# Optimization experiments

Measured on AMD Instinct MI355X. Metric: run time of the kernel, lower is better.

Reference implementation:

```python
import jax, jax.numpy as jnp
import numpy as np

N_NODES = 100000
N_EDGES = 1600000
IN_F = 256
OUT_F = 64


def setup_inputs() -> dict:
    key = jax.random.key(0)
    k1, k2, k3, k4, k5, k6 = jax.random.split(key, 6)
    x = jax.random.normal(k1, (N_NODES, IN_F), dtype=jnp.float32)
    edge_vals = jax.random.uniform(k2, (N_EDGES,), dtype=jnp.float32)
    W = jax.random.normal(k3, (IN_F, OUT_F), dtype=jnp.float32) * (1.0 / np.sqrt(OUT_F))
    bias = jax.random.normal(k4, (OUT_F,), dtype=jnp.float32) * (1.0 / np.sqrt(OUT_F))
    row_idx = jnp.sort(jax.random.randint(k5, (N_EDGES,), 0, N_NODES, dtype=jnp.int32))
    col_idx = jax.random.randint(k6, (N_EDGES,), 0, N_NODES, dtype=jnp.int32)
    return {"x": x, "edge_vals": edge_vals, "W": W, "bias": bias,
            "row_idx": row_idx, "col_idx": col_idx}


def reference(x, edge_vals, W, bias, row_idx, col_idx):
    # support = X @ W  (dense GEMM; torch.mm / torch.spmm branch)
    support = x @ W                                  # [N, OUT_F]
    # flexspmm: output = A @ support, A given as weighted edge list
    msgs = support[col_idx] * edge_vals[:, None]      # [E, OUT_F] gather + scale
    out = jax.ops.segment_sum(msgs, row_idx, num_segments=x.shape[0])  # [N, OUT_F]
    return out + bias
```

## Files before the change

kernel.cpp:

```cpp
#include <hip/hip_runtime.h>
#include <hip/hip_bf16.h>

#define N_NODES 100000
#define N_EDGES 1600000
#define IN_F 256
#define OUT_F 64

typedef short bf16x8 __attribute__((ext_vector_type(8)));
typedef float f32x4 __attribute__((ext_vector_type(4)));

__device__ __forceinline__ short f2bf(float f) {
  unsigned u = __float_as_uint(f);
  u += 0x7FFF + ((u >> 16) & 1);
  return (short)(u >> 16);
}
__device__ __forceinline__ float bf2f(unsigned short u) {
  return __uint_as_float(((unsigned)u) << 16);
}

__global__ __launch_bounds__(256) void build_row_ptr_kernel(
    const int* __restrict__ row_idx, int* __restrict__ row_ptr) {
  int i = blockIdx.x * blockDim.x + threadIdx.x;
  if (i > N_NODES) return;
  int lo = 0, hi = N_EDGES;
  while (lo < hi) {
    int mid = (lo + hi) >> 1;
    if (row_idx[mid] < i) lo = mid + 1; else hi = mid;
  }
  row_ptr[i] = lo;
}

__global__ __launch_bounds__(256) void wfrag_kernel(
    const float* __restrict__ W, short* __restrict__ Wf) {
  int tid = blockIdx.x * blockDim.x + threadIdx.x;
  if (tid >= 2048) return;
  int s = tid >> 8;
  int r = tid & 255;
  int t = r >> 6;
  int lane = r & 63;
  int col = t * 16 + (lane & 15);
  int kbase = s * 32 + ((lane >> 4) & 3) * 8;
#pragma unroll
  for (int j = 0; j < 8; ++j) {
    Wf[(size_t)tid * 8 + j] = f2bf(W[(size_t)(kbase + j) * OUT_F + col]);
  }
}

__global__ __launch_bounds__(256) void gemm_kernel(
    const float* __restrict__ x, const short* __restrict__ Wf,
    unsigned short* __restrict__ supB) {
  __shared__ short sWf[8 * 4 * 64 * 8];
  {
    const float4* g = reinterpret_cast<const float4*>(Wf);
    float4* s4 = reinterpret_cast<float4*>(sWf);
#pragma unroll
    for (int i = 0; i < 8; ++i) s4[threadIdx.x + i * 256] = g[threadIdx.x + i * 256];
  }
  __syncthreads();

  const int lane = threadIdx.x & 63;
  const int wave = threadIdx.x >> 6;
  const int r0_base = blockIdx.x * 64 + wave * 16;

  int arow = r0_base + (lane & 15);
  if (arow >= N_NODES) arow = N_NODES - 1;
  const float* xrow = x + (size_t)arow * IN_F + ((lane >> 4) & 3) * 8;

  f32x4 acc0 = {0.f, 0.f, 0.f, 0.f};
  f32x4 acc1 = {0.f, 0.f, 0.f, 0.f};
  f32x4 acc2 = {0.f, 0.f, 0.f, 0.f};
  f32x4 acc3 = {0.f, 0.f, 0.f, 0.f};

#pragma unroll
  for (int s = 0; s < 8; ++s) {
    const float4 f0 = *reinterpret_cast<const float4*>(xrow + s * 32);
    const float4 f1 = *reinterpret_cast<const float4*>(xrow + s * 32 + 4);
    bf16x8 a;
    a[0] = f2bf(f0.x); a[1] = f2bf(f0.y); a[2] = f2bf(f0.z); a[3] = f2bf(f0.w);
    a[4] = f2bf(f1.x); a[5] = f2bf(f1.y); a[6] = f2bf(f1.z); a[7] = f2bf(f1.w);
    const bf16x8 b0 = *reinterpret_cast<const bf16x8*>(&sWf[((s * 4 + 0) * 64 + lane) * 8]);
    const bf16x8 b1 = *reinterpret_cast<const bf16x8*>(&sWf[((s * 4 + 1) * 64 + lane) * 8]);
    const bf16x8 b2 = *reinterpret_cast<const bf16x8*>(&sWf[((s * 4 + 2) * 64 + lane) * 8]);
    const bf16x8 b3 = *reinterpret_cast<const bf16x8*>(&sWf[((s * 4 + 3) * 64 + lane) * 8]);
    acc0 = __builtin_amdgcn_mfma_f32_16x16x32_bf16(a, b0, acc0, 0, 0, 0);
    acc1 = __builtin_amdgcn_mfma_f32_16x16x32_bf16(a, b1, acc1, 0, 0, 0);
    acc2 = __builtin_amdgcn_mfma_f32_16x16x32_bf16(a, b2, acc2, 0, 0, 0);
    acc3 = __builtin_amdgcn_mfma_f32_16x16x32_bf16(a, b3, acc3, 0, 0, 0);
  }

  const int orow_base = r0_base + ((lane >> 4) & 3) * 4;
  const int ocol = lane & 15;
#pragma unroll
  for (int r = 0; r < 4; ++r) {
    const int row = orow_base + r;
    if (row < N_NODES) {
      unsigned short* o = supB + (size_t)row * OUT_F + ocol;
      o[0]  = (unsigned short)f2bf(acc0[r]);
      o[16] = (unsigned short)f2bf(acc1[r]);
      o[32] = (unsigned short)f2bf(acc2[r]);
      o[48] = (unsigned short)f2bf(acc3[r]);
    }
  }
}

__global__ __launch_bounds__(256) void spmm_kernel(
    const unsigned short* __restrict__ supB, const float* __restrict__ ev,
    const int* __restrict__ col, const int* __restrict__ row_ptr,
    const float* __restrict__ bias, float* __restrict__ out) {
  const int lane = threadIdx.x & 63;
  const int g = lane >> 4;
  const int fq = lane & 15;
  const int gwave = (blockIdx.x * blockDim.x + threadIdx.x) >> 6;
  const int nwaves = (gridDim.x * blockDim.x) >> 6;

  const float b0 = bias[fq * 4 + 0];
  const float b1 = bias[fq * 4 + 1];
  const float b2 = bias[fq * 4 + 2];
  const float b3 = bias[fq * 4 + 3];

  for (int node = gwave; node < N_NODES; node += nwaves) {
    const int s = row_ptr[node];
    const int e = row_ptr[node + 1];
    float a0 = 0.f, a1 = 0.f, a2 = 0.f, a3 = 0.f;

    for (int i = s; i < e; i += 8) {
      const int i0 = i + g;
      const int i1 = i + 4 + g;
      const bool p0 = i0 < e;
      const bool p1 = i1 < e;
      const int c0 = p0 ? col[i0] : 0;
      const int c1 = p1 ? col[i1] : 0;
      const float v0 = p0 ? ev[i0] : 0.f;
      const float v1 = p1 ? ev[i1] : 0.f;
      const ushort4 s0 = *reinterpret_cast<const ushort4*>(supB + (size_t)c0 * OUT_F + fq * 4);
      const ushort4 s1 = *reinterpret_cast<const ushort4*>(supB + (size_t)c1 * OUT_F + fq * 4);
      a0 = fmaf(v0, bf2f(s0.x), a0);
      a1 = fmaf(v0, bf2f(s0.y), a1);
      a2 = fmaf(v0, bf2f(s0.z), a2);
      a3 = fmaf(v0, bf2f(s0.w), a3);
      a0 = fmaf(v1, bf2f(s1.x), a0);
      a1 = fmaf(v1, bf2f(s1.y), a1);
      a2 = fmaf(v1, bf2f(s1.z), a2);
      a3 = fmaf(v1, bf2f(s1.w), a3);
    }

    a0 += __shfl_xor(a0, 16); a0 += __shfl_xor(a0, 32);
    a1 += __shfl_xor(a1, 16); a1 += __shfl_xor(a1, 32);
    a2 += __shfl_xor(a2, 16); a2 += __shfl_xor(a2, 32);
    a3 += __shfl_xor(a3, 16); a3 += __shfl_xor(a3, 32);

    if (lane < 16) {
      float4 o;
      o.x = a0 + b0; o.y = a1 + b1; o.z = a2 + b2; o.w = a3 + b3;
      *reinterpret_cast<float4*>(out + (size_t)node * OUT_F + fq * 4) = o;
    }
  }
}

extern "C" void kernel_launch(void* const* d_in, const int* in_sizes, int n_in,
                              void* d_out, int out_size, void* d_ws, size_t ws_size,
                              hipStream_t stream) {
  const float* x        = (const float*)d_in[0];
  const float* ev       = (const float*)d_in[1];
  const float* W        = (const float*)d_in[2];
  const float* bias     = (const float*)d_in[3];
  const int*   row_idx  = (const int*)d_in[4];
  const int*   col_idx  = (const int*)d_in[5];
  float* out = (float*)d_out;

  int*            row_ptr = (int*)d_ws;
  short*          Wf      = (short*)((char*)d_ws + 448 * 1024);
  unsigned short* supB    = (unsigned short*)((char*)d_ws + 512 * 1024);

  build_row_ptr_kernel<<<(N_NODES + 1 + 255) / 256, 256, 0, stream>>>(row_idx, row_ptr);
  wfrag_kernel<<<8, 256, 0, stream>>>(W, Wf);

  gemm_kernel<<<(N_NODES + 63) / 64, 256, 0, stream>>>(x, Wf, supB);

  spmm_kernel<<<2048, 256, 0, stream>>>(supB, ev, col_idx, row_ptr, bias, out);
}
```

Baseline: 79.44 us.

## Process two nodes per wave iteration with contiguous node ranges and nontemporal loads

The SpMM kernel now gives each wave a contiguous block of nodes instead of a strided assignment. It processes two adjacent rows at once, interleaving their edge loops so more independent gathers are in flight per iteration. It also reuses the row_ptr boundary between consecutive rows. Streaming loads of col/ev and x in the GEMM, and the output stores, are marked nontemporal so they do not pollute cache needed for the gathered support rows. Pairing rows of unequal length wastes lanes on predicated-off slots.

After: 104.3 us. +31.3%, slower.

```diff
diff --git a/kernel.cpp b/kernel.cpp
--- a/kernel.cpp
+++ b/kernel.cpp
@@ -8,6 +8,7 @@
 
 typedef short bf16x8 __attribute__((ext_vector_type(8)));
 typedef float f32x4 __attribute__((ext_vector_type(4)));
+typedef unsigned short u16x4 __attribute__((ext_vector_type(4)));
 
 __device__ __forceinline__ short f2bf(float f) {
   unsigned u = __float_as_uint(f);
@@ -73,11 +74,13 @@
 
 #pragma unroll
   for (int s = 0; s < 8; ++s) {
-    const float4 f0 = *reinterpret_cast<const float4*>(xrow + s * 32);
-    const float4 f1 = *reinterpret_cast<const float4*>(xrow + s * 32 + 4);
+    const f32x4 f0 = __builtin_nontemporal_load(
+        reinterpret_cast<const f32x4*>(xrow + s * 32));
+    const f32x4 f1 = __builtin_nontemporal_load(
+        reinterpret_cast<const f32x4*>(xrow + s * 32 + 4));
     bf16x8 a;
-    a[0] = f2bf(f0.x); a[1] = f2bf(f0.y); a[2] = f2bf(f0.z); a[3] = f2bf(f0.w);
-    a[4] = f2bf(f1.x); a[5] = f2bf(f1.y); a[6] = f2bf(f1.z); a[7] = f2bf(f1.w);
+    a[0] = f2bf(f0[0]); a[1] = f2bf(f0[1]); a[2] = f2bf(f0[2]); a[3] = f2bf(f0[3]);
+    a[4] = f2bf(f1[0]); a[5] = f2bf(f1[1]); a[6] = f2bf(f1[2]); a[7] = f2bf(f1[3]);
     const bf16x8 b0 = *reinterpret_cast<const bf16x8*>(&sWf[((s * 4 + 0) * 64 + lane) * 8]);
     const bf16x8 b1 = *reinterpret_cast<const bf16x8*>(&sWf[((s * 4 + 1) * 64 + lane) * 8]);
     const bf16x8 b2 = *reinterpret_cast<const bf16x8*>(&sWf[((s * 4 + 2) * 64 + lane) * 8]);
@@ -113,47 +116,78 @@
   const int gwave = (blockIdx.x * blockDim.x + threadIdx.x) >> 6;
   const int nwaves = (gridDim.x * blockDim.x) >> 6;
 
+  const int per = (N_NODES + nwaves - 1) / nwaves;
+  const int n0 = gwave * per;
+  if (n0 >= N_NODES) return;
+  const int n1 = (n0 + per < N_NODES) ? n0 + per : N_NODES;
+
   const float b0 = bias[fq * 4 + 0];
   const float b1 = bias[fq * 4 + 1];
   const float b2 = bias[fq * 4 + 2];
   const float b3 = bias[fq * 4 + 3];
 
-  for (int node = gwave; node < N_NODES; node += nwaves) {
-    const int s = row_ptr[node];
-    const int e = row_ptr[node + 1];
-    float a0 = 0.f, a1 = 0.f, a2 = 0.f, a3 = 0.f;
-
-    for (int i = s; i < e; i += 8) {
-      const int i0 = i + g;
-      const int i1 = i + 4 + g;
-      const bool p0 = i0 < e;
-      const bool p1 = i1 < e;
-      const int c0 = p0 ? col[i0] : 0;
-      const int c1 = p1 ? col[i1] : 0;
-      const float v0 = p0 ? ev[i0] : 0.f;
-      const float v1 = p1 ? ev[i1] : 0.f;
-      const ushort4 s0 = *reinterpret_cast<const ushort4*>(supB + (size_t)c0 * OUT_F + fq * 4);
-      const ushort4 s1 = *reinterpret_cast<const ushort4*>(supB + (size_t)c1 * OUT_F + fq * 4);
-      a0 = fmaf(v0, bf2f(s0.x), a0);
-      a1 = fmaf(v0, bf2f(s0.y), a1);
-      a2 = fmaf(v0, bf2f(s0.z), a2);
-      a3 = fmaf(v0, bf2f(s0.w), a3);
-      a0 = fmaf(v1, bf2f(s1.x), a0);
-      a1 = fmaf(v1, bf2f(s1.y), a1);
-      a2 = fmaf(v1, bf2f(s1.z), a2);
-      a3 = fmaf(v1, bf2f(s1.w), a3);
+  int sA = row_ptr[n0];
+  for (int nn = n0; nn < n1; nn += 2) {
+    const bool hasB = (nn + 1 < n1);
+    const int m  = row_ptr[nn + 1];
+    const int eB = hasB ? row_ptr[nn + 2] : m;
+
+    float aA0 = 0.f, aA1 = 0.f, aA2 = 0.f, aA3 = 0.f;
+    float aB0 = 0.f, aB1 = 0.f, aB2 = 0.f, aB3 = 0.f;
+
+    int iA = sA, iB = m;
+    while (iA < m || iB < eB) {
+      const int a0i = iA + g,     a1i = iA + 4 + g;
+      const int b0i = iB + g,     b1i = iB + 4 + g;
+      const bool pa0 = a0i < m,   pa1 = a1i < m;
+      const bool pb0 = b0i < eB,  pb1 = b1i < eB;
+
+      const int   ca0 = pa0 ? __builtin_nontemporal_load(col + a0i) : 0;
+      const int   ca1 = pa1 ? __builtin_nontemporal_load(col + a1i) : 0;
+      const int   cb0 = pb0 ? __builtin_nontemporal_load(col + b0i) : 0;
+      const int   cb1 = pb1 ? __builtin_nontemporal_load(col + b1i) : 0;
+      const float va0 = pa0 ? __builtin_nontemporal_load(ev + a0i) : 0.f;
+      const float va1 = pa1 ? __builtin_nontemporal_load(ev + a1i) : 0.f;
+      const float vb0 = pb0 ? __builtin_nontemporal_load(ev + b0i) : 0.f;
+      const float vb1 = pb1 ? __builtin_nontemporal_load(ev + b1i) : 0.f;
+
+      const u16x4 sa0 = *reinterpret_cast<const u16x4*>(supB + (size_t)ca0 * OUT_F + fq * 4);
+      const u16x4 sa1 = *reinterpret_cast<const u16x4*>(supB + (size_t)ca1 * OUT_F + fq * 4);
+      const u16x4 sb0 = *reinterpret_cast<const u16x4*>(supB + (size_t)cb0 * OUT_F + fq * 4);
+      const u16x4 sb1 = *reinterpret_cast<const u16x4*>(supB + (size_t)cb1 * OUT_F + fq * 4);
+
+      aA0 = fmaf(va0, bf2f(sa0[0]), aA0); aA0 = fmaf(va1, bf2f(sa1[0]), aA0);
+      aA1 = fmaf(va0, bf2f(sa0[1]), aA1); aA1 = fmaf(va1, bf2f(sa1[1]), aA1);
+      aA2 = fmaf(va0, bf2f(sa0[2]), aA2); aA2 = fmaf(va1, bf2f(sa1[2]), aA2);
+      aA3 = fmaf(va0, bf2f(sa0[3]), aA3); aA3 = fmaf(va1, bf2f(sa1[3]), aA3);
+      aB0 = fmaf(vb0, bf2f(sb0[0]), aB0); aB0 = fmaf(vb1, bf2f(sb1[0]), aB0);
+      aB1 = fmaf(vb0, bf2f(sb0[1]), aB1); aB1 = fmaf(vb1, bf2f(sb1[1]), aB1);
+      aB2 = fmaf(vb0, bf2f(sb0[2]), aB2); aB2 = fmaf(vb1, bf2f(sb1[2]), aB2);
+      aB3 = fmaf(vb0, bf2f(sb0[3]), aB3); aB3 = fmaf(vb1, bf2f(sb1[3]), aB3);
+
+      iA += 8; iB += 8;
     }
 
-    a0 += __shfl_xor(a0, 16); a0 += __shfl_xor(a0, 32);
-    a1 += __shfl_xor(a1, 16); a1 += __shfl_xor(a1, 32);
-    a2 += __shfl_xor(a2, 16); a2 += __shfl_xor(a2, 32);
-    a3 += __shfl_xor(a3, 16); a3 += __shfl_xor(a3, 32);
+    aA0 += __shfl_xor(aA0, 16); aA0 += __shfl_xor(aA0, 32);
+    aA1 += __shfl_xor(aA1, 16); aA1 += __shfl_xor(aA1, 32);
+    aA2 += __shfl_xor(aA2, 16); aA2 += __shfl_xor(aA2, 32);
+    aA3 += __shfl_xor(aA3, 16); aA3 += __shfl_xor(aA3, 32);
+    aB0 += __shfl_xor(aB0, 16); aB0 += __shfl_xor(aB0, 32);
+    aB1 += __shfl_xor(aB1, 16); aB1 += __shfl_xor(aB1, 32);
+    aB2 += __shfl_xor(aB2, 16); aB2 += __shfl_xor(aB2, 32);
+    aB3 += __shfl_xor(aB3, 16); aB3 += __shfl_xor(aB3, 32);
 
     if (lane < 16) {
-      float4 o;
-      o.x = a0 + b0; o.y = a1 + b1; o.z = a2 + b2; o.w = a3 + b3;
-      *reinterpret_cast<float4*>(out + (size_t)node * OUT_F + fq * 4) = o;
+      f32x4 oA = {aA0 + b0, aA1 + b1, aA2 + b2, aA3 + b3};
+      __builtin_nontemporal_store(
+          oA, reinterpret_cast<f32x4*>(out + (size_t)nn * OUT_F + fq * 4));
+      if (hasB) {
+        f32x4 oB = {aB0 + b0, aB1 + b1, aB2 + b2, aB3 + b3};
+        __builtin_nontemporal_store(
+            oB, reinterpret_cast<f32x4*>(out + (size_t)(nn + 1) * OUT_F + fq * 4));
+      }
     }
+    sA = eB;
   }
 }
 
```
